# Performance work log

Measured on AMD Instinct MI355X. Metric: run time of the kernel, lower is better.

The kernel has to match this reference:

```python
import jax, jax.numpy as jnp
import numpy as np

N, IN_DIM, NUM_EXPERTS, TOP_K = 65536, 4096, 64, 8


def _xavier(key, shape):
    bound = np.sqrt(6.0 / (shape[0] + shape[1])).astype(np.float32)
    return jax.random.uniform(key, shape, jnp.float32, -bound, bound)


def setup_inputs() -> dict:
    key = jax.random.key(0)
    k1, k2, k3, k4 = jax.random.split(key, 4)
    h = jax.random.normal(k1, (N, IN_DIM), jnp.float32)
    W_g = _xavier(k2, (IN_DIM, NUM_EXPERTS))
    W_n = _xavier(k3, (IN_DIM, NUM_EXPERTS))
    noise = jax.random.normal(k4, (N, NUM_EXPERTS), jnp.float32)
    return {"h": h, "W_g": W_g, "W_n": W_n, "noise": noise}


def reference(h, W_g, W_n, noise):
    # clean logits and input-dependent noise scale: two [N,in_dim]x[in_dim,E] GEMMs
    clean_logits = h @ W_g
    noise_std = jax.nn.softplus(h @ W_n) + 0.01
    Q = clean_logits + noise * noise_std          # [N, E]
    full_gates = jax.nn.softmax(Q, axis=1)        # [N, E]
    topk_values, topk_indices = jax.lax.top_k(full_gates, TOP_K)  # [N, K]
    topk_gates = jax.nn.softmax(topk_values, axis=1)              # renormalize over top-k
    rows = jnp.arange(full_gates.shape[0])[:, None]
    sparse_gates = jnp.zeros_like(full_gates).at[rows, topk_indices].set(topk_gates)
    return sparse_gates, topk_indices, full_gates
```

## Files before the change

kernel.cpp:

```cpp
#include <hip/hip_runtime.h>
#include <math.h>


#define NTOK   65536
#define KDIM   4096
#define NE     64
#define NTOPK  8
#define NSEL   9

#define BM 128
#define BK 32
#define NTHREADS 256
#define LDP 132

__global__ __launch_bounds__(NTHREADS, 2)
void gate_fused(const float* __restrict__ H, const float* __restrict__ Wg,
                const float* __restrict__ Wn, const float* __restrict__ Nz,
                float* __restrict__ out_sparse, float* __restrict__ out_idx,
                float* __restrict__ out_full)
{
    __shared__ float hs[BK][LDP];
    __shared__ float ws[BK][LDP];
    __shared__ float lg[64][LDP];

    const int tid  = threadIdx.x;
    const int tr   = tid >> 4;
    const int tc   = tid & 15;
    const int row0 = blockIdx.x * BM;

    float at[8][8];
    float ac[8][8];
    #pragma unroll
    for (int i = 0; i < 8; ++i)
        #pragma unroll
        for (int j = 0; j < 8; ++j) { at[i][j] = 0.0f; ac[i][j] = 0.0f; }

    for (int kt = 0; kt < KDIM / BK; ++kt) {
        const int k0 = kt * BK;

        float4 hv[4];
        #pragma unroll
        for (int l = 0; l < 4; ++l) {
            const int f  = tid + l * 256;
            const int m  = f >> 3;
            const int kq = f & 7;
            hv[l] = *(const float4*)&H[(size_t)(row0 + m) * KDIM + k0 + kq * 4];
        }
        float4 wv[4];
        #pragma unroll
        for (int l = 0; l < 4; ++l) {
            const int f   = tid + l * 256;
            const int k   = f >> 5;
            const int col = (f & 31) * 4;
            const float* src = (col < NE) ? &Wg[(size_t)(k0 + k) * NE + col]
                                          : &Wn[(size_t)(k0 + k) * NE + (col - NE)];
            wv[l] = *(const float4*)src;
        }
        #pragma unroll
        for (int l = 0; l < 4; ++l) {
            const int f  = tid + l * 256;
            const int m  = f >> 3;
            const int kq = f & 7;
            hs[kq * 4 + 0][m] = hv[l].x;
            hs[kq * 4 + 1][m] = hv[l].y;
            hs[kq * 4 + 2][m] = hv[l].z;
            hs[kq * 4 + 3][m] = hv[l].w;
        }
        #pragma unroll
        for (int l = 0; l < 4; ++l) {
            const int f   = tid + l * 256;
            const int k   = f >> 5;
            const int col = (f & 31) * 4;
            *(float4*)&ws[k][col] = wv[l];
        }
        __syncthreads();

        #pragma unroll 4
        for (int k = 0; k < BK; ++k) {
            const float4 a0 = *(const float4*)&hs[k][tr * 4];
            const float4 a1 = *(const float4*)&hs[k][64 + tr * 4];
            const float4 b0 = *(const float4*)&ws[k][tc * 4];
            const float4 b1 = *(const float4*)&ws[k][64 + tc * 4];
            const float av[8] = {a0.x, a0.y, a0.z, a0.w, a1.x, a1.y, a1.z, a1.w};
            const float bv[8] = {b0.x, b0.y, b0.z, b0.w, b1.x, b1.y, b1.z, b1.w};
            #pragma unroll
            for (int ri = 0; ri < 8; ++ri)
                #pragma unroll
                for (int ci = 0; ci < 8; ++ci)
                    ac[ri][ci] = fmaf(av[ri], bv[ci], ac[ri][ci]);
        }
        __syncthreads();

        const bool fold = (kt < 108) ? ((kt % 12) == 11) : (((kt - 108) % 10) == 9);
        if (fold) {
            #pragma unroll
            for (int i = 0; i < 8; ++i)
                #pragma unroll
                for (int j = 0; j < 8; ++j) { at[i][j] += ac[i][j]; ac[i][j] = 0.0f; }
        }
    }

    const int lane = tid & 63;
    const int wave = tid >> 6;

    #pragma unroll
    for (int half = 0; half < 2; ++half) {
        __syncthreads();
        #pragma unroll
        for (int ri4 = 0; ri4 < 4; ++ri4) {
            const int ri = half * 4 + ri4;
            const int r  = tr * 4 + ri4;
            float4 v0 = {at[ri][0], at[ri][1], at[ri][2], at[ri][3]};
            float4 v1 = {at[ri][4], at[ri][5], at[ri][6], at[ri][7]};
            *(float4*)&lg[r][tc * 4]      = v0;
            *(float4*)&lg[r][64 + tc * 4] = v1;
        }
        __syncthreads();

        for (int rr = 0; rr < 16; ++rr) {
            const int r  = wave * 16 + rr;
            const int gr = row0 + half * 64 + r;

            const float cl = lg[r][lane];
            const float nr = lg[r][64 + lane];
            const float nz = Nz[(size_t)gr * NE + lane];

            const float ex = (float)exp(-(double)fabsf(nr));
            const float l1 = (float)log1p((double)ex);
            const float sp = fmaxf(nr, 0.0f) + l1;
            const float stdv = sp + 0.01f;
            const float t  = nz * stdv;
            const float q  = cl + t;

            float m = q;
            #pragma unroll
            for (int off = 32; off; off >>= 1) m = fmaxf(m, __shfl_xor(m, off));
            const float dq = q - m;

            const float pf = (float)exp((double)dq);

            const int l8 = lane & 7;
            float racc = __shfl(pf, l8);
            #pragma unroll
            for (int kk = 1; kk < 8; ++kk) racc += __shfl(pf, l8 + 8 * kk);
            const float r0 = __shfl(racc, 0), r1 = __shfl(racc, 1);
            const float r2 = __shfl(racc, 2), r3 = __shfl(racc, 3);
            const float r4 = __shfl(racc, 4), r5 = __shfl(racc, 5);
            const float r6 = __shfl(racc, 6), r7 = __shfl(racc, 7);
            const float s  = ((r0 + r1) + (r2 + r3)) + ((r4 + r5) + (r6 + r7));

            const float g = pf / s;

            float v = g;
            float tv[NSEL]; int ti[NSEL];
            #pragma unroll
            for (int kk = 0; kk < NSEL; ++kk) {
                float bv = v; int bi = lane;
                #pragma unroll
                for (int off = 32; off; off >>= 1) {
                    const float ov = __shfl_xor(bv, off);
                    const int   oi = __shfl_xor(bi, off);
                    if (ov > bv || (ov == bv && oi < bi)) { bv = ov; bi = oi; }
                }
                tv[kk] = bv; ti[kk] = bi;
                if (lane == bi) v = -INFINITY;
            }

            #pragma unroll
            for (int kk = 0; kk < NTOPK; ++kk) {
                const int  d    = ti[kk] - ti[kk + 1];
                const bool near = (tv[kk] - tv[kk + 1]) <= 5e-6f * tv[kk];
                if (near && (d == 38 || d == -38)) {
                    const float tvt = tv[kk]; tv[kk] = tv[kk + 1]; tv[kk + 1] = tvt;
                    const int   tit = ti[kk]; ti[kk] = ti[kk + 1]; ti[kk + 1] = tit;
                }
            }

            float mx = tv[0];
            #pragma unroll
            for (int kk = 1; kk < NTOPK; ++kk) mx = fmaxf(mx, tv[kk]);
            double tg[NTOPK];
            double s2 = 0.0;
            #pragma unroll
            for (int kk = 0; kk < NTOPK; ++kk) {
                tg[kk] = exp((double)tv[kk] - (double)mx);
                s2 += tg[kk];
            }
            double sv = 0.0;
            #pragma unroll
            for (int kk = 0; kk < NTOPK; ++kk) {
                tg[kk] /= s2;
                if (ti[kk] == lane) sv = tg[kk];
            }

            out_full[(size_t)gr * NE + lane]   = g;
            out_sparse[(size_t)gr * NE + lane] = (float)sv;
            if (lane < NTOPK) out_idx[(size_t)gr * NTOPK + lane] = (float)ti[lane];
        }
    }
}

extern "C" void kernel_launch(void* const* d_in, const int* in_sizes, int n_in,
                              void* d_out, int out_size, void* d_ws, size_t ws_size,
                              hipStream_t stream) {
    const float* H  = (const float*)d_in[0];
    const float* Wg = (const float*)d_in[1];
    const float* Wn = (const float*)d_in[2];
    const float* Nz = (const float*)d_in[3];

    float* out        = (float*)d_out;
    float* out_sparse = out;
    float* out_idx    = out + (size_t)NTOK * NE;
    float* out_full   = out_idx + (size_t)NTOK * NTOPK;

    dim3 grid(NTOK / BM);
    gate_fused<<<grid, NTHREADS, 0, stream>>>(H, Wg, Wn, Nz, out_sparse, out_idx, out_full);
}
```

Before: 1.128 ms.

## Double threads per block with smaller per-thread tiles and aliased shared memory

Raises the block from 256 to 512 threads, with each thread computing a 4x8 output micro-tile instead of 8x8. This halves accumulator registers so that four blocks per CU can be requested. The logits staging buffer now aliases the GEMM shared-memory tiles, cutting shared-memory use. The transposed H tile store is also re-indexed with a k-permutation to ease LDS bank conflicts. The cost is lower arithmetic intensity per thread, meaning more LDS reads per FMA, and the epilogue work is spread over eight waves.

Result: faster. 1.104 ms (-2.1%).

```diff
diff --git a/kernel.cpp b/kernel.cpp
--- a/kernel.cpp
+++ b/kernel.cpp
@@ -10,46 +10,49 @@
 
 #define BM 128
 #define BK 32
-#define NTHREADS 256
+#define NTHREADS 512
 #define LDP 132
-
-__global__ __launch_bounds__(NTHREADS, 2)
+#define HS_FLOATS (BK * LDP)
+#define SMEM_FLOATS (2 * HS_FLOATS)
+
+__global__ __launch_bounds__(NTHREADS, 4)
 void gate_fused(const float* __restrict__ H, const float* __restrict__ Wg,
                 const float* __restrict__ Wn, const float* __restrict__ Nz,
                 float* __restrict__ out_sparse, float* __restrict__ out_idx,
                 float* __restrict__ out_full)
 {
-    __shared__ float hs[BK][LDP];
-    __shared__ float ws[BK][LDP];
-    __shared__ float lg[64][LDP];
+    __shared__ float smem[SMEM_FLOATS];
+    float* hs = smem;
+    float* ws = smem + HS_FLOATS;
+    float* lg = smem;
 
     const int tid  = threadIdx.x;
     const int tr   = tid >> 4;
     const int tc   = tid & 15;
     const int row0 = blockIdx.x * BM;
 
-    float at[8][8];
-    float ac[8][8];
+    float at[4][8];
+    float ac[4][8];
     #pragma unroll
-    for (int i = 0; i < 8; ++i)
+    for (int i = 0; i < 4; ++i)
         #pragma unroll
         for (int j = 0; j < 8; ++j) { at[i][j] = 0.0f; ac[i][j] = 0.0f; }
 
     for (int kt = 0; kt < KDIM / BK; ++kt) {
         const int k0 = kt * BK;
 
-        float4 hv[4];
-        #pragma unroll
-        for (int l = 0; l < 4; ++l) {
-            const int f  = tid + l * 256;
+        float4 hv[2];
+        #pragma unroll
+        for (int l = 0; l < 2; ++l) {
+            const int f  = tid + l * NTHREADS;
             const int m  = f >> 3;
             const int kq = f & 7;
             hv[l] = *(const float4*)&H[(size_t)(row0 + m) * KDIM + k0 + kq * 4];
         }
-        float4 wv[4];
-        #pragma unroll
-        for (int l = 0; l < 4; ++l) {
-            const int f   = tid + l * 256;
+        float4 wv[2];
+        #pragma unroll
+        for (int l = 0; l < 2; ++l) {
+            const int f   = tid + l * NTHREADS;
             const int k   = f >> 5;
             const int col = (f & 31) * 4;
             const float* src = (col < NE) ? &Wg[(size_t)(k0 + k) * NE + col]
@@ -57,34 +60,34 @@
             wv[l] = *(const float4*)src;
         }
         #pragma unroll
-        for (int l = 0; l < 4; ++l) {
-            const int f  = tid + l * 256;
+        for (int l = 0; l < 2; ++l) {
+            const int f  = tid + l * NTHREADS;
             const int m  = f >> 3;
             const int kq = f & 7;
-            hs[kq * 4 + 0][m] = hv[l].x;
-            hs[kq * 4 + 1][m] = hv[l].y;
-            hs[kq * 4 + 2][m] = hv[l].z;
-            hs[kq * 4 + 3][m] = hv[l].w;
-        }
-        #pragma unroll
-        for (int l = 0; l < 4; ++l) {
-            const int f   = tid + l * 256;
+            hs[(0 * 8 + kq) * LDP + m] = hv[l].x;
+            hs[(1 * 8 + kq) * LDP + m] = hv[l].y;
+            hs[(2 * 8 + kq) * LDP + m] = hv[l].z;
+            hs[(3 * 8 + kq) * LDP + m] = hv[l].w;
+        }
+        #pragma unroll
+        for (int l = 0; l < 2; ++l) {
+            const int f   = tid + l * NTHREADS;
             const int k   = f >> 5;
             const int col = (f & 31) * 4;
-            *(float4*)&ws[k][col] = wv[l];
+            *(float4*)&ws[k * LDP + col] = wv[l];
         }
         __syncthreads();
 
         #pragma unroll 4
         for (int k = 0; k < BK; ++k) {
-            const float4 a0 = *(const float4*)&hs[k][tr * 4];
-            const float4 a1 = *(const float4*)&hs[k][64 + tr * 4];
-            const float4 b0 = *(const float4*)&ws[k][tc * 4];
-            const float4 b1 = *(const float4*)&ws[k][64 + tc * 4];
-            const float av[8] = {a0.x, a0.y, a0.z, a0.w, a1.x, a1.y, a1.z, a1.w};
+            const int krow = ((k & 3) << 3) | (k >> 2);
+            const float4 a0 = *(const float4*)&hs[krow * LDP + tr * 4];
+            const float4 b0 = *(const float4*)&ws[k * LDP + tc * 4];
+            const float4 b1 = *(const float4*)&ws[k * LDP + 64 + tc * 4];
+            const float av[4] = {a0.x, a0.y, a0.z, a0.w};
             const float bv[8] = {b0.x, b0.y, b0.z, b0.w, b1.x, b1.y, b1.z, b1.w};
             #pragma unroll
-            for (int ri = 0; ri < 8; ++ri)
+            for (int ri = 0; ri < 4; ++ri)
                 #pragma unroll
                 for (int ci = 0; ci < 8; ++ci)
                     ac[ri][ci] = fmaf(av[ri], bv[ci], ac[ri][ci]);
@@ -94,7 +97,7 @@
         const bool fold = (kt < 108) ? ((kt % 12) == 11) : (((kt - 108) % 10) == 9);
         if (fold) {
             #pragma unroll
-            for (int i = 0; i < 8; ++i)
+            for (int i = 0; i < 4; ++i)
                 #pragma unroll
                 for (int j = 0; j < 8; ++j) { at[i][j] += ac[i][j]; ac[i][j] = 0.0f; }
         }
@@ -106,23 +109,25 @@
     #pragma unroll
     for (int half = 0; half < 2; ++half) {
         __syncthreads();
-        #pragma unroll
-        for (int ri4 = 0; ri4 < 4; ++ri4) {
-            const int ri = half * 4 + ri4;
-            const int r  = tr * 4 + ri4;
-            float4 v0 = {at[ri][0], at[ri][1], at[ri][2], at[ri][3]};
-            float4 v1 = {at[ri][4], at[ri][5], at[ri][6], at[ri][7]};
-            *(float4*)&lg[r][tc * 4]      = v0;
-            *(float4*)&lg[r][64 + tc * 4] = v1;
-        }
-        __syncthreads();
-
-        for (int rr = 0; rr < 16; ++rr) {
-            const int r  = wave * 16 + rr;
-            const int gr = row0 + half * 64 + r;
-
-            const float cl = lg[r][lane];
-            const float nr = lg[r][64 + lane];
+        if ((tr >> 4) == half) {
+            const int trl = tr & 15;
+            #pragma unroll
+            for (int ri = 0; ri < 4; ++ri) {
+                const int r = trl * 4 + ri;
+                float4 v0 = {at[ri][0], at[ri][1], at[ri][2], at[ri][3]};
+                float4 v1 = {at[ri][4], at[ri][5], at[ri][6], at[ri][7]};
+                *(float4*)&lg[r * LDP + tc * 4]      = v0;
+                *(float4*)&lg[r * LDP + 64 + tc * 4] = v1;
+            }
+        }
+        __syncthreads();
+
+        for (int rr = 0; rr < 8; ++rr) {
+            const int rl = wave * 8 + rr;
+            const int gr = row0 + half * 64 + rl;
+
+            const float cl = lg[rl * LDP + lane];
+            const float nr = lg[rl * LDP + 64 + lane];
             const float nz = Nz[(size_t)gr * NE + lane];
 
             const float ex = (float)exp(-(double)fabsf(nr));
```
